# Kernel tuning notes

Measured on AMD Instinct MI355X. Metric: run time of the kernel, lower is better.

## Reference

```python
import jax, jax.numpy as jnp
import numpy as np

N = 100_000
E = 1_600_000
D_IN = 128
D_HID = 128
D_OUT = 16
K = 3  # PyG TAGConv default number of hops


def setup_inputs() -> dict:
    key = jax.random.key(0)
    ks = jax.random.split(key, 5)
    x = jax.random.normal(ks[0], (N, D_IN), dtype=jnp.float32)
    edge_index = jax.random.randint(ks[1], (2, E), 0, N, dtype=jnp.int32)
    # TAGConv has (K+1) bias-free linear layers + one shared bias per conv
    W1 = jax.random.normal(ks[2], (K + 1, D_IN, D_HID), dtype=jnp.float32) * 0.05
    b1 = jnp.zeros((D_HID,), dtype=jnp.float32)
    W2 = jax.random.normal(ks[3], (K + 1, D_HID, D_OUT), dtype=jnp.float32) * 0.05
    b2 = jnp.zeros((D_OUT,), dtype=jnp.float32)
    return {"x": x, "edge_index": edge_index, "W1": W1, "b1": b1, "W2": W2, "b2": b2}


def _tag_conv(x, src, dst, norm, W, b):
    # out = sum_{k=0..K} (A_norm^k x) @ W[k] + b
    out = x @ W[0]
    h = x
    for k in range(1, W.shape[0]):
        msg = h[src] * norm[:, None]                      # [E, d] gather
        h = jax.ops.segment_sum(msg, dst, num_segments=x.shape[0])  # scatter-add
        out = out + h @ W[k]
    return out + b


def reference(x, edge_index, W1, b1, W2, b2):
    src, dst = edge_index[0], edge_index[1]
    # gcn_norm without self-loops: deg over target nodes
    deg = jax.ops.segment_sum(jnp.ones((src.shape[0],), x.dtype), dst, num_segments=x.shape[0])
    dis = jnp.where(deg > 0, jax.lax.rsqrt(jnp.maximum(deg, 1.0)), 0.0).astype(x.dtype)
    norm = dis[src] * dis[dst]
    h = jax.nn.relu(_tag_conv(x, src, dst, norm, W1, b1))
    return _tag_conv(h, src, dst, norm, W2, b2)
```

## Files before the change

kernel.cpp:

```cpp
#include <hip/hip_runtime.h>

#define DF 128

typedef __attribute__((ext_vector_type(8))) short bf16x8;
typedef __attribute__((ext_vector_type(4))) float f32x4;

__device__ __forceinline__ ushort f2bf(float f) {
  uint u = __float_as_uint(f);
  u += 0x7fff + ((u >> 16) & 1);
  return (ushort)(u >> 16);
}
__device__ __forceinline__ float bfl(uint v) { return __uint_as_float(v << 16); }
__device__ __forceinline__ float bfh(uint v) { return __uint_as_float(v & 0xffff0000u); }
__device__ __forceinline__ float b2f(ushort s) { return __uint_as_float(((uint)s) << 16); }

__global__ __launch_bounds__(256) void prepw_k(const float* __restrict__ W1, const float* __restrict__ W2,
                                               ushort* __restrict__ W1f, ushort* __restrict__ W2f,
                                               ushort* __restrict__ Z3s, ushort* __restrict__ T,
                                               ushort* __restrict__ GBs3, ushort* __restrict__ F0,
                                               ushort* __restrict__ F1, int n) {
  int b = blockIdx.x, tid = threadIdx.x;
  if (b == 256) {
    if (tid < 128) {
      Z3s[(size_t)n * 128 + tid] = 0;
      T[(size_t)n * 128 + tid] = 0;
    }
    if (tid < 16) {
      GBs3[(size_t)n * 16 + tid] = 0;
      F0[(size_t)n * 16 + tid] = 0;
      F1[(size_t)n * 16 + tid] = 0;
    }
    return;
  }
  int t = b * 256 + tid;
  {
    int k = t >> 14, rem = t & 16383;
    int frag = rem >> 3, j = rem & 7;
    int nt = frag >> 8, ks = (frag >> 6) & 3, lane = frag & 63;
    int nn = nt * 16 + (lane & 15);
    int kk = ks * 32 + (lane >> 4) * 8 + j;
    W1f[t] = f2bf(W1[k * 16384 + kk * 128 + nn]);
  }
  if (t < 8192) {
    int frag = t >> 3, j = t & 7;
    int nt = frag >> 8, ks = (frag >> 6) & 3, lane = frag & 63;
    int kk = ks * 32 + (lane >> 4) * 8 + j;
    W2f[t] = f2bf(W2[nt * 2048 + kk * 16 + (lane & 15)]);
  }
}

__global__ __launch_bounds__(256) void k1_k(const float* __restrict__ x, const ushort* __restrict__ W1f,
                                            ushort* __restrict__ Z3, ushort* __restrict__ Z2,
                                            ushort* __restrict__ Z1, ushort* __restrict__ Z0,
                                            const int* __restrict__ dst, int e,
                                            int* __restrict__ deg_s, int* __restrict__ rank,
                                            int n, int GZ) {
  int b = blockIdx.x, tid = threadIdx.x;
  if (b >= GZ) {
    int i = (b - GZ) * 256 + tid;
    if (i < e) {
      int shard = (i >> 8) & 7;
      rank[i] = atomicAdd(&deg_s[(size_t)shard * n + dst[i]], 1);
    }
    return;
  }
  int wid = tid >> 6, lane = tid & 63;
  int l15 = lane & 15, kgrp = lane >> 4;
  int m0 = b * 128 + wid * 32 + l15;
  int m1 = m0 + 16;
  int mc0 = m0 < n ? m0 : n - 1;
  int mc1 = m1 < n ? m1 : n - 1;
  bf16x8 xf0[4], xf1[4];
#pragma unroll
  for (int ks = 0; ks < 4; ks++) {
    float4 a0 = *reinterpret_cast<const float4*>(x + (size_t)mc0 * 128 + ks * 32 + kgrp * 8);
    float4 a1 = *reinterpret_cast<const float4*>(x + (size_t)mc0 * 128 + ks * 32 + kgrp * 8 + 4);
    float4 b0 = *reinterpret_cast<const float4*>(x + (size_t)mc1 * 128 + ks * 32 + kgrp * 8);
    float4 b1v = *reinterpret_cast<const float4*>(x + (size_t)mc1 * 128 + ks * 32 + kgrp * 8 + 4);
    bf16x8 u, w;
    u[0] = (short)f2bf(a0.x); u[1] = (short)f2bf(a0.y); u[2] = (short)f2bf(a0.z); u[3] = (short)f2bf(a0.w);
    u[4] = (short)f2bf(a1.x); u[5] = (short)f2bf(a1.y); u[6] = (short)f2bf(a1.z); u[7] = (short)f2bf(a1.w);
    w[0] = (short)f2bf(b0.x); w[1] = (short)f2bf(b0.y); w[2] = (short)f2bf(b0.z); w[3] = (short)f2bf(b0.w);
    w[4] = (short)f2bf(b1v.x); w[5] = (short)f2bf(b1v.y); w[6] = (short)f2bf(b1v.z); w[7] = (short)f2bf(b1v.w);
    xf0[ks] = u; xf1[ks] = w;
  }
#pragma unroll
  for (int kk = 0; kk < 4; kk++) {
    const int k = 3 - kk;
    const ushort* Wk = W1f + (size_t)k * 16384;
    ushort* Out = (k == 3) ? Z3 : (k == 2) ? Z2 : (k == 1) ? Z1 : Z0;
#pragma unroll
    for (int nt = 0; nt < 8; nt++) {
      f32x4 acc0 = {0.f, 0.f, 0.f, 0.f}, acc1 = {0.f, 0.f, 0.f, 0.f};
#pragma unroll
      for (int ks = 0; ks < 4; ks++) {
        bf16x8 wf = *reinterpret_cast<const bf16x8*>(Wk + (size_t)((nt * 4 + ks) * 64 + lane) * 8);
        acc0 = __builtin_amdgcn_mfma_f32_16x16x32_bf16(wf, xf0[ks], acc0, 0, 0, 0);
        acc1 = __builtin_amdgcn_mfma_f32_16x16x32_bf16(wf, xf1[ks], acc1, 0, 0, 0);
      }
      int ncol = nt * 16 + kgrp * 4;
      if (m0 < n) {
        ushort4 st; st.x = f2bf(acc0[0]); st.y = f2bf(acc0[1]);
        st.z = f2bf(acc0[2]); st.w = f2bf(acc0[3]);
        *reinterpret_cast<ushort4*>(Out + (size_t)m0 * 128 + ncol) = st;
      }
      if (m1 < n) {
        ushort4 st; st.x = f2bf(acc1[0]); st.y = f2bf(acc1[1]);
        st.z = f2bf(acc1[2]); st.w = f2bf(acc1[3]);
        *reinterpret_cast<ushort4*>(Out + (size_t)m1 * 128 + ncol) = st;
      }
    }
  }
}

__global__ __launch_bounds__(256) void reduce_k(const int* __restrict__ deg_s, int n,
                                                int* __restrict__ deg, int* __restrict__ P,
                                                float* __restrict__ dis) {
  int i = blockIdx.x * 256 + threadIdx.x;
  if (i >= n) return;
  int run = 0;
#pragma unroll
  for (int s = 0; s < 8; s++) {
    int v = deg_s[(size_t)s * n + i];
    P[(size_t)s * n + i] = run;
    run += v;
  }
  deg[i] = run;
  dis[i] = run > 0 ? rsqrtf((float)run) : 0.f;
}

__global__ __launch_bounds__(256) void scan1_k(const int* __restrict__ deg, int n, int* __restrict__ partials) {
  __shared__ int sm[256];
  int base = blockIdx.x * 1024;
  int s = 0;
#pragma unroll
  for (int j = 0; j < 4; j++) { int idx = base + threadIdx.x * 4 + j; if (idx < n) s += deg[idx]; }
  sm[threadIdx.x] = s; __syncthreads();
  for (int off = 128; off > 0; off >>= 1) {
    if (threadIdx.x < off) sm[threadIdx.x] += sm[threadIdx.x + off];
    __syncthreads();
  }
  if (threadIdx.x == 0) partials[blockIdx.x] = sm[0];
}

__global__ void scan2_k(int* partials, int nb) {
  if (threadIdx.x == 0 && blockIdx.x == 0) {
    int run = 0;
    for (int i = 0; i < nb; i++) { int v = partials[i]; partials[i] = run; run += v; }
  }
}

__global__ __launch_bounds__(256) void scan3_k(const int* __restrict__ deg, int n, int e,
                                               const int* __restrict__ partials,
                                               int* __restrict__ rowptr) {
  __shared__ int sm[256];
  int base = blockIdx.x * 1024;
  int loc[4]; int s = 0;
#pragma unroll
  for (int j = 0; j < 4; j++) {
    int idx = base + threadIdx.x * 4 + j;
    int v = (idx < n) ? deg[idx] : 0;
    loc[j] = s; s += v;
  }
  sm[threadIdx.x] = s; __syncthreads();
  int tsum = s;
  for (int off = 1; off < 256; off <<= 1) {
    int v = (threadIdx.x >= (unsigned)off) ? sm[threadIdx.x - off] : 0;
    __syncthreads();
    sm[threadIdx.x] += v;
    __syncthreads();
  }
  int excl = sm[threadIdx.x] - tsum + partials[blockIdx.x];
#pragma unroll
  for (int j = 0; j < 4; j++) {
    int idx = base + threadIdx.x * 4 + j;
    if (idx < n) rowptr[idx] = excl + loc[j];
  }
  if (blockIdx.x == 0 && threadIdx.x == 0) rowptr[n] = e;
}

__global__ __launch_bounds__(256) void k2_k(const int* __restrict__ src, const int* __restrict__ dst, int e,
                                            const int* __restrict__ rank, const int* __restrict__ rowptr,
                                            const int* __restrict__ P, int* __restrict__ colb,
                                            ushort* __restrict__ Z3, const float* __restrict__ dis,
                                            int n, int gE) {
  int b = blockIdx.x, tid = threadIdx.x;
  if (b < gE) {
    int i = b * 256 + tid;
    if (i < e) {
      int d = dst[i];
      int shard = (i >> 8) & 7;
      int p = rowptr[d] + P[(size_t)shard * n + d] + rank[i];
      colb[p] = src[i];
    }
  } else {
    int u = (b - gE) * 256 + tid;
    int i = u >> 4, seg = u & 15;
    if (i < n) {
      float d = dis[i];
      ushort* p = Z3 + (size_t)i * 128 + seg * 8;
      uint4 v = *reinterpret_cast<const uint4*>(p);
      uint4 o;
      o.x = (uint)f2bf(d * bfl(v.x)) | ((uint)f2bf(d * bfh(v.x)) << 16);
      o.y = (uint)f2bf(d * bfl(v.y)) | ((uint)f2bf(d * bfh(v.y)) << 16);
      o.z = (uint)f2bf(d * bfl(v.z)) | ((uint)f2bf(d * bfh(v.z)) << 16);
      o.w = (uint)f2bf(d * bfl(v.w)) | ((uint)f2bf(d * bfh(v.w)) << 16);
      *reinterpret_cast<uint4*>(p) = o;
    }
  }
}

__global__ __launch_bounds__(256) void hop_k(const ushort* __restrict__ hin, const ushort* __restrict__ zk,
                                             const float* __restrict__ b1, ushort* __restrict__ hout,
                                             const int* __restrict__ rowptr, const int* __restrict__ colb,
                                             const float* __restrict__ dis, int n, int colhalf, int last) {
  int node = blockIdx.x * 16 + (threadIdx.x >> 4);
  int gl = threadIdx.x & 15;
  if (node >= n) return;
  int cbase = colhalf * 64 + gl * 4;
  int e0 = rowptr[node], e1 = rowptr[node + 1];
  float a0 = 0.f, a1 = 0.f, a2 = 0.f, a3 = 0.f;
  for (int ee = e0; ee < e1; ee += 8) {
    int c[8];
#pragma unroll
    for (int j = 0; j < 8; j++) {
      int idx = ee + j;
      c[j] = idx < e1 ? colb[idx] : n;
    }
    uint2 v[8];
#pragma unroll
    for (int j = 0; j < 8; j++)
      v[j] = *reinterpret_cast<const uint2*>(hin + (size_t)c[j] * 128 + cbase);
#pragma unroll
    for (int j = 0; j < 8; j++) {
      a0 += bfl(v[j].x); a1 += bfh(v[j].x);
      a2 += bfl(v[j].y); a3 += bfh(v[j].y);
    }
  }
  float d = dis[node];
  uint2 zr = *reinterpret_cast<const uint2*>(zk + (size_t)node * 128 + cbase);
  float t0 = fmaf(d, a0, bfl(zr.x)), t1 = fmaf(d, a1, bfh(zr.x));
  float t2 = fmaf(d, a2, bfl(zr.y)), t3 = fmaf(d, a3, bfh(zr.y));
  uint2 st;
  if (last) {
    float4 bv = *reinterpret_cast<const float4*>(b1 + cbase);
    t0 = fmaxf(t0 + bv.x, 0.f); t1 = fmaxf(t1 + bv.y, 0.f);
    t2 = fmaxf(t2 + bv.z, 0.f); t3 = fmaxf(t3 + bv.w, 0.f);
    st.x = (uint)f2bf(t0) | ((uint)f2bf(t1) << 16);
    st.y = (uint)f2bf(t2) | ((uint)f2bf(t3) << 16);
  } else {
    st.x = (uint)f2bf(d * t0) | ((uint)f2bf(d * t1) << 16);
    st.y = (uint)f2bf(d * t2) | ((uint)f2bf(d * t3) << 16);
  }
  *reinterpret_cast<uint2*>(hout + (size_t)node * 128 + cbase) = st;
}

__global__ __launch_bounds__(256) void gemm_last_k(const ushort* __restrict__ h1, const ushort* __restrict__ W2f,
                                                   const float* __restrict__ dis,
                                                   ushort* __restrict__ GB, ushort* __restrict__ GBs3, int n) {
  int wid = threadIdx.x >> 6, lane = threadIdx.x & 63;
  int kgrp = lane >> 4;
  int m = blockIdx.x * 64 + wid * 16 + (lane & 15);
  int mc = m < n ? m : n - 1;
  float dm = dis[mc];
  bf16x8 xf[4];
#pragma unroll
  for (int ks = 0; ks < 4; ks++)
    xf[ks] = *reinterpret_cast<const bf16x8*>(h1 + (size_t)mc * 128 + ks * 32 + kgrp * 8);
#pragma unroll
  for (int nt = 0; nt < 4; nt++) {
    f32x4 acc = {0.f, 0.f, 0.f, 0.f};
#pragma unroll
    for (int ks = 0; ks < 4; ks++) {
      bf16x8 wf = *reinterpret_cast<const bf16x8*>(W2f + (size_t)((nt * 4 + ks) * 64 + lane) * 8);
      acc = __builtin_amdgcn_mfma_f32_16x16x32_bf16(wf, xf[ks], acc, 0, 0, 0);
    }
    if (m < n) {
      int ncol = nt * 16 + kgrp * 4;
      ushort4 st; st.x = f2bf(acc[0]); st.y = f2bf(acc[1]); st.z = f2bf(acc[2]); st.w = f2bf(acc[3]);
      *reinterpret_cast<ushort4*>(GB + (size_t)m * 64 + ncol) = st;
      if (nt == 3) {
        ushort4 ss; ss.x = f2bf(dm * acc[0]); ss.y = f2bf(dm * acc[1]);
        ss.z = f2bf(dm * acc[2]); ss.w = f2bf(dm * acc[3]);
        *reinterpret_cast<ushort4*>(GBs3 + (size_t)m * 16 + kgrp * 4) = ss;
      }
    }
  }
}

__global__ __launch_bounds__(256) void spmm16_k(const ushort* __restrict__ in,
                                                const ushort* __restrict__ addraw, int addstride,
                                                const float* __restrict__ b2,
                                                float* __restrict__ outf, ushort* __restrict__ outb,
                                                const int* __restrict__ rowptr, const int* __restrict__ colb,
                                                const float* __restrict__ dis, int n) {
  int t = blockIdx.x * 256 + threadIdx.x;
  int node = t >> 3, cp = t & 7;
  if (node >= n) return;
  int e0 = rowptr[node], e1 = rowptr[node + 1];
  float a0 = 0.f, a1 = 0.f;
  for (int ee = e0; ee < e1; ee += 4) {
    int c[4];
#pragma unroll
    for (int j = 0; j < 4; j++) {
      int idx = ee + j;
      c[j] = idx < e1 ? colb[idx] : n;
    }
    uint v[4];
#pragma unroll
    for (int j = 0; j < 4; j++)
      v[j] = *reinterpret_cast<const uint*>(in + (size_t)c[j] * 16 + cp * 2);
#pragma unroll
    for (int j = 0; j < 4; j++) { a0 += bfl(v[j]); a1 += bfh(v[j]); }
  }
  float d = dis[node];
  uint av = *reinterpret_cast<const uint*>(addraw + (size_t)node * addstride + cp * 2);
  float t0 = fmaf(d, a0, b2f((ushort)(av & 0xffff)));
  float t1 = fmaf(d, a1, b2f((ushort)(av >> 16)));
  if (outf) {
    float2 st; st.x = t0 + b2[cp * 2]; st.y = t1 + b2[cp * 2 + 1];
    *reinterpret_cast<float2*>(outf + (size_t)node * 16 + cp * 2) = st;
  } else {
    uint pk = (uint)f2bf(d * t0) | ((uint)f2bf(d * t1) << 16);
    *reinterpret_cast<uint*>(outb + (size_t)node * 16 + cp * 2) = pk;
  }
}

extern "C" void kernel_launch(void* const* d_in, const int* in_sizes, int n_in,
                              void* d_out, int out_size, void* d_ws, size_t ws_size,
                              hipStream_t stream) {
  const float* x  = (const float*)d_in[0];
  const int*   ei = (const int*)d_in[1];
  const float* W1 = (const float*)d_in[2];
  const float* b1 = (const float*)d_in[3];
  const float* W2 = (const float*)d_in[4];
  const float* b2 = (const float*)d_in[5];
  float* out = (float*)d_out;

  const int n = in_sizes[0] / DF;
  const int e = in_sizes[1] / 2;
  const int* srcp = ei;
  const int* dstp = ei + e;

  char* ws = (char*)d_ws;
  size_t off = 0;
  auto alloc = [&](size_t bytes) -> void* {
    void* p = ws + off;
    off += (bytes + 255) & ~(size_t)255;
    return p;
  };
  ushort* Z3s  = (ushort*)alloc((size_t)(n + 1) * 128 * 2);
  ushort* T    = (ushort*)alloc((size_t)(n + 1) * 128 * 2);
  ushort* Z2   = (ushort*)alloc((size_t)n * 128 * 2);
  ushort* Z1   = (ushort*)alloc((size_t)n * 128 * 2);
  ushort* Z0   = (ushort*)alloc((size_t)n * 128 * 2);
  int*   deg_s = (int*)alloc((size_t)8 * n * 4);
  int*   P     = (int*)alloc((size_t)8 * n * 4);
  int*   deg   = (int*)alloc((size_t)n * 4);
  float* dis   = (float*)alloc((size_t)n * 4);
  int*   rowptr= (int*)alloc((size_t)(n + 1) * 4);
  int*   rank  = (int*)alloc((size_t)e * 4);
  int*   partials = (int*)alloc(1024 * 4);
  int*   colb  = (int*)alloc((size_t)e * 4);
  ushort* W1f  = (ushort*)alloc(4 * 128 * 128 * 2);
  ushort* W2f  = (ushort*)alloc(64 * 128 * 2);
  ushort* GBs3 = (ushort*)alloc((size_t)(n + 1) * 16 * 2);
  ushort* F0   = (ushort*)alloc((size_t)(n + 1) * 16 * 2);
  ushort* F1   = (ushort*)alloc((size_t)(n + 1) * 16 * 2);
  ushort* Up = Z3s;
  ushort* h1 = T;
  ushort* GB = Z2;

  hipMemsetAsync(deg_s, 0, (size_t)8 * n * 4, stream);

  int gE = (e + 255) / 256;
  int gN = (n + 255) / 256;
  int nb = (n + 1023) / 1024;
  int GZ = (n + 127) / 128;

  prepw_k<<<257, 256, 0, stream>>>(W1, W2, W1f, W2f, Z3s, T, GBs3, F0, F1, n);
  k1_k<<<GZ + gE, 256, 0, stream>>>(x, W1f, Z3s, Z2, Z1, Z0, dstp, e, deg_s, rank, n, GZ);
  reduce_k<<<gN, 256, 0, stream>>>(deg_s, n, deg, P, dis);
  scan1_k<<<nb, 256, 0, stream>>>(deg, n, partials);
  scan2_k<<<1, 64, 0, stream>>>(partials, nb);
  scan3_k<<<nb, 256, 0, stream>>>(deg, n, e, partials, rowptr);
  int gScale = (n * 16 + 255) / 256;
  k2_k<<<gE + gScale, 256, 0, stream>>>(srcp, dstp, e, rank, rowptr, P, colb, Z3s, dis, n, gE);

  int gHop = (n + 15) / 16;
  int gGemm = (n + 63) / 64;
  int gS16 = (n * 8 + 255) / 256;

  hop_k<<<gHop, 256, 0, stream>>>(Z3s, Z2, nullptr, T, rowptr, colb, dis, n, 0, 0);
  hop_k<<<gHop, 256, 0, stream>>>(Z3s, Z2, nullptr, T, rowptr, colb, dis, n, 1, 0);
  hop_k<<<gHop, 256, 0, stream>>>(T, Z1, nullptr, Up, rowptr, colb, dis, n, 0, 0);
  hop_k<<<gHop, 256, 0, stream>>>(T, Z1, nullptr, Up, rowptr, colb, dis, n, 1, 0);
  hop_k<<<gHop, 256, 0, stream>>>(Up, Z0, b1, h1, rowptr, colb, dis, n, 0, 1);
  hop_k<<<gHop, 256, 0, stream>>>(Up, Z0, b1, h1, rowptr, colb, dis, n, 1, 1);
  gemm_last_k<<<gGemm, 256, 0, stream>>>(h1, W2f, dis, GB, GBs3, n);

  spmm16_k<<<gS16, 256, 0, stream>>>(GBs3, GB + 32, 64, nullptr, nullptr, F0, rowptr, colb, dis, n);
  spmm16_k<<<gS16, 256, 0, stream>>>(F0,   GB + 16, 64, nullptr, nullptr, F1, rowptr, colb, dis, n);
  spmm16_k<<<gS16, 256, 0, stream>>>(F1,   GB + 0,  64, b2, out, nullptr, rowptr, colb, dis, n);
}
```

Measured before the change: 404.7 us.

## Interleave degree atomics with GEMM blocks, stage weights in LDS, fuse reduce+scan1

```diff
diff --git a/kernel.cpp b/kernel.cpp
--- a/kernel.cpp
+++ b/kernel.cpp
@@ -13,6 +13,11 @@
 __device__ __forceinline__ float bfl(uint v) { return __uint_as_float(v << 16); }
 __device__ __forceinline__ float bfh(uint v) { return __uint_as_float(v & 0xffff0000u); }
 __device__ __forceinline__ float b2f(ushort s) { return __uint_as_float(((uint)s) << 16); }
+
+__device__ __forceinline__ void gload16(const ushort* g, ushort* l) {
+  __builtin_amdgcn_global_load_lds((const __attribute__((address_space(1))) void*)g,
+                                   (__attribute__((address_space(3))) void*)l, 16, 0, 0);
+}
 
 __global__ __launch_bounds__(256) void prepw_k(const float* __restrict__ W1, const float* __restrict__ W2,
                                                ushort* __restrict__ W1f, ushort* __restrict__ W2f,
@@ -55,92 +60,125 @@
                                             const int* __restrict__ dst, int e,
                                             int* __restrict__ deg_s, int* __restrict__ rank,
                                             int n, int GZ) {
+  __shared__ ushort wbuf[16384];
   int b = blockIdx.x, tid = threadIdx.x;
-  if (b >= GZ) {
-    int i = (b - GZ) * 256 + tid;
-    if (i < e) {
+
+  int ebase = b * 2048 + tid;
+  int mydst[8], myrank[8];
+#pragma unroll
+  for (int j = 0; j < 8; j++) {
+    int i = ebase + j * 256;
+    mydst[j] = (i < e) ? dst[i] : -1;
+  }
+#pragma unroll
+  for (int j = 0; j < 8; j++) {
+    int i = ebase + j * 256;
+    if (mydst[j] >= 0) {
       int shard = (i >> 8) & 7;
-      rank[i] = atomicAdd(&deg_s[(size_t)shard * n + dst[i]], 1);
-    }
-    return;
-  }
-  int wid = tid >> 6, lane = tid & 63;
-  int l15 = lane & 15, kgrp = lane >> 4;
-  int m0 = b * 128 + wid * 32 + l15;
-  int m1 = m0 + 16;
-  int mc0 = m0 < n ? m0 : n - 1;
-  int mc1 = m1 < n ? m1 : n - 1;
-  bf16x8 xf0[4], xf1[4];
-#pragma unroll
-  for (int ks = 0; ks < 4; ks++) {
-    float4 a0 = *reinterpret_cast<const float4*>(x + (size_t)mc0 * 128 + ks * 32 + kgrp * 8);
-    float4 a1 = *reinterpret_cast<const float4*>(x + (size_t)mc0 * 128 + ks * 32 + kgrp * 8 + 4);
-    float4 b0 = *reinterpret_cast<const float4*>(x + (size_t)mc1 * 128 + ks * 32 + kgrp * 8);
-    float4 b1v = *reinterpret_cast<const float4*>(x + (size_t)mc1 * 128 + ks * 32 + kgrp * 8 + 4);
-    bf16x8 u, w;
-    u[0] = (short)f2bf(a0.x); u[1] = (short)f2bf(a0.y); u[2] = (short)f2bf(a0.z); u[3] = (short)f2bf(a0.w);
-    u[4] = (short)f2bf(a1.x); u[5] = (short)f2bf(a1.y); u[6] = (short)f2bf(a1.z); u[7] = (short)f2bf(a1.w);
-    w[0] = (short)f2bf(b0.x); w[1] = (short)f2bf(b0.y); w[2] = (short)f2bf(b0.z); w[3] = (short)f2bf(b0.w);
-    w[4] = (short)f2bf(b1v.x); w[5] = (short)f2bf(b1v.y); w[6] = (short)f2bf(b1v.z); w[7] = (short)f2bf(b1v.w);
-    xf0[ks] = u; xf1[ks] = w;
-  }
-#pragma unroll
-  for (int kk = 0; kk < 4; kk++) {
-    const int k = 3 - kk;
-    const ushort* Wk = W1f + (size_t)k * 16384;
-    ushort* Out = (k == 3) ? Z3 : (k == 2) ? Z2 : (k == 1) ? Z1 : Z0;
-#pragma unroll
-    for (int nt = 0; nt < 8; nt++) {
-      f32x4 acc0 = {0.f, 0.f, 0.f, 0.f}, acc1 = {0.f, 0.f, 0.f, 0.f};
+      myrank[j] = atomicAdd(&deg_s[(size_t)shard * n + mydst[j]], 1);
+    }
+  }
+
+  if (b < GZ) {
+    int wid = tid >> 6, lane = tid & 63;
+    int l15 = lane & 15, kgrp = lane >> 4;
+    int m0 = b * 128 + wid * 32 + l15;
+    int m1 = m0 + 16;
+    int mc0 = m0 < n ? m0 : n - 1;
+    int mc1 = m1 < n ? m1 : n - 1;
+    bf16x8 xf0[4], xf1[4];
+#pragma unroll
+    for (int ks = 0; ks < 4; ks++) {
+      float4 a0 = *reinterpret_cast<const float4*>(x + (size_t)mc0 * 128 + ks * 32 + kgrp * 8);
+      float4 a1 = *reinterpret_cast<const float4*>(x + (size_t)mc0 * 128 + ks * 32 + kgrp * 8 + 4);
+      float4 b0 = *reinterpret_cast<const float4*>(x + (size_t)mc1 * 128 + ks * 32 + kgrp * 8);
+      float4 b1v = *reinterpret_cast<const float4*>(x + (size_t)mc1 * 128 + ks * 32 + kgrp * 8 + 4);
+      bf16x8 u, w;
+      u[0] = (short)f2bf(a0.x); u[1] = (short)f2bf(a0.y); u[2] = (short)f2bf(a0.z); u[3] = (short)f2bf(a0.w);
+      u[4] = (short)f2bf(a1.x); u[5] = (short)f2bf(a1.y); u[6] = (short)f2bf(a1.z); u[7] = (short)f2bf(a1.w);
+      w[0] = (short)f2bf(b0.x); w[1] = (short)f2bf(b0.y); w[2] = (short)f2bf(b0.z); w[3] = (short)f2bf(b0.w);
+      w[4] = (short)f2bf(b1v.x); w[5] = (short)f2bf(b1v.y); w[6] = (short)f2bf(b1v.z); w[7] = (short)f2bf(b1v.w);
+      xf0[ks] = u; xf1[ks] = w;
+    }
+#pragma unroll
+    for (int kk = 0; kk < 4; kk++) {
+      const int k = 3 - kk;
+      {
+        const ushort* gsrc = W1f + (size_t)k * 16384;
+#pragma unroll
+        for (int it = 0; it < 8; it++) {
+          int f = it * 256 + tid;
+          gload16(gsrc + (size_t)f * 8, &wbuf[f * 8]);
+        }
+      }
+      __syncthreads();
+      f32x4 acc0[8], acc1[8];
+#pragma unroll
+      for (int nt = 0; nt < 8; nt++) { acc0[nt] = {0.f,0.f,0.f,0.f}; acc1[nt] = {0.f,0.f,0.f,0.f}; }
 #pragma unroll
       for (int ks = 0; ks < 4; ks++) {
-        bf16x8 wf = *reinterpret_cast<const bf16x8*>(Wk + (size_t)((nt * 4 + ks) * 64 + lane) * 8);
-        acc0 = __builtin_amdgcn_mfma_f32_16x16x32_bf16(wf, xf0[ks], acc0, 0, 0, 0);
-        acc1 = __builtin_amdgcn_mfma_f32_16x16x32_bf16(wf, xf1[ks], acc1, 0, 0, 0);
+#pragma unroll
+        for (int nt = 0; nt < 8; nt++) {
+          bf16x8 wf = *reinterpret_cast<const bf16x8*>(&wbuf[((nt * 4 + ks) * 64 + lane) * 8]);
+          acc0[nt] = __builtin_amdgcn_mfma_f32_16x16x32_bf16(wf, xf0[ks], acc0[nt], 0, 0, 0);
+          acc1[nt] = __builtin_amdgcn_mfma_f32_16x16x32_bf16(wf, xf1[ks], acc1[nt], 0, 0, 0);
+        }
       }
-      int ncol = nt * 16 + kgrp * 4;
-      if (m0 < n) {
-        ushort4 st; st.x = f2bf(acc0[0]); st.y = f2bf(acc0[1]);
-        st.z = f2bf(acc0[2]); st.w = f2bf(acc0[3]);
-        *reinterpret_cast<ushort4*>(Out + (size_t)m0 * 128 + ncol) = st;
+      ushort* Out = (k == 3) ? Z3 : (k == 2) ? Z2 : (k == 1) ? Z1 : Z0;
+#pragma unroll
+      for (int nt = 0; nt < 8; nt++) {
+        int ncol = nt * 16 + kgrp * 4;
+        if (m0 < n) {
+          ushort4 st; st.x = f2bf(acc0[nt][0]); st.y = f2bf(acc0[nt][1]);
+          st.z = f2bf(acc0[nt][2]); st.w = f2bf(acc0[nt][3]);
+          *reinterpret_cast<ushort4*>(Out + (size_t)m0 * 128 + ncol) = st;
+        }
+        if (m1 < n) {
+          ushort4 st; st.x = f2bf(acc1[nt][0]); st.y = f2bf(acc1[nt][1]);
+          st.z = f2bf(acc1[nt][2]); st.w = f2bf(acc1[nt][3]);
+          *reinterpret_cast<ushort4*>(Out + (size_t)m1 * 128 + ncol) = st;
+        }
       }
-      if (m1 < n) {
-        ushort4 st; st.x = f2bf(acc1[0]); st.y = f2bf(acc1[1]);
-        st.z = f2bf(acc1[2]); st.w = f2bf(acc1[3]);
-        *reinterpret_cast<ushort4*>(Out + (size_t)m1 * 128 + ncol) = st;
-      }
-    }
-  }
-}
-
-__global__ __launch_bounds__(256) void reduce_k(const int* __restrict__ deg_s, int n,
-                                                int* __restrict__ deg, int* __restrict__ P,
-                                                float* __restrict__ dis) {
-  int i = blockIdx.x * 256 + threadIdx.x;
-  if (i >= n) return;
-  int run = 0;
-#pragma unroll
-  for (int s = 0; s < 8; s++) {
-    int v = deg_s[(size_t)s * n + i];
-    P[(size_t)s * n + i] = run;
-    run += v;
-  }
-  deg[i] = run;
-  dis[i] = run > 0 ? rsqrtf((float)run) : 0.f;
-}
-
-__global__ __launch_bounds__(256) void scan1_k(const int* __restrict__ deg, int n, int* __restrict__ partials) {
+      __syncthreads();
+    }
+  }
+
+#pragma unroll
+  for (int j = 0; j < 8; j++) {
+    int i = ebase + j * 256;
+    if (i < e) rank[i] = myrank[j];
+  }
+}
+
+__global__ __launch_bounds__(256) void rs1_k(const int* __restrict__ deg_s, int n,
+                                             int* __restrict__ deg, int* __restrict__ P,
+                                             float* __restrict__ dis, int* __restrict__ partials) {
   __shared__ int sm[256];
+  int tid = threadIdx.x;
   int base = blockIdx.x * 1024;
   int s = 0;
 #pragma unroll
-  for (int j = 0; j < 4; j++) { int idx = base + threadIdx.x * 4 + j; if (idx < n) s += deg[idx]; }
-  sm[threadIdx.x] = s; __syncthreads();
+  for (int j = 0; j < 4; j++) {
+    int idx = base + tid * 4 + j;
+    if (idx < n) {
+      int run = 0;
+#pragma unroll
+      for (int sh = 0; sh < 8; sh++) {
+        int v = deg_s[(size_t)sh * n + idx];
+        P[(size_t)sh * n + idx] = run;
+        run += v;
+      }
+      deg[idx] = run;
+      dis[idx] = run > 0 ? rsqrtf((float)run) : 0.f;
+      s += run;
+    }
+  }
+  sm[tid] = s; __syncthreads();
   for (int off = 128; off > 0; off >>= 1) {
-    if (threadIdx.x < off) sm[threadIdx.x] += sm[threadIdx.x + off];
+    if (tid < off) sm[tid] += sm[tid + off];
     __syncthreads();
   }
-  if (threadIdx.x == 0) partials[blockIdx.x] = sm[0];
+  if (tid == 0) partials[blockIdx.x] = sm[0];
 }
 
 __global__ void scan2_k(int* partials, int nb) {
@@ -374,14 +412,14 @@
   hipMemsetAsync(deg_s, 0, (size_t)8 * n * 4, stream);
 
   int gE = (e + 255) / 256;
-  int gN = (n + 255) / 256;
   int nb = (n + 1023) / 1024;
   int GZ = (n + 127) / 128;
+  long covered = (long)GZ * 2048;
+  int EX = covered >= e ? 0 : (int)((e - covered + 2047) / 2048);
 
   prepw_k<<<257, 256, 0, stream>>>(W1, W2, W1f, W2f, Z3s, T, GBs3, F0, F1, n);
-  k1_k<<<GZ + gE, 256, 0, stream>>>(x, W1f, Z3s, Z2, Z1, Z0, dstp, e, deg_s, rank, n, GZ);
-  reduce_k<<<gN, 256, 0, stream>>>(deg_s, n, deg, P, dis);
-  scan1_k<<<nb, 256, 0, stream>>>(deg, n, partials);
+  k1_k<<<GZ + EX, 256, 0, stream>>>(x, W1f, Z3s, Z2, Z1, Z0, dstp, e, deg_s, rank, n, GZ);
+  rs1_k<<<nb, 256, 0, stream>>>(deg_s, n, deg, P, dis, partials);
   scan2_k<<<1, 64, 0, stream>>>(partials, nb);
   scan3_k<<<nb, 256, 0, stream>>>(deg, n, e, partials, rowptr);
   int gScale = (n * 16 + 255) / 256;
```

Result: slower. 418.0 us (+3.3%).
